# Optimization experiments

Measured on AMD Instinct MI355X. Metric: run time of the kernel, lower is better.

Reference implementation:

```python
import jax, jax.numpy as jnp
import numpy as np
from jax import lax

LENGTH = 9
PAD = LENGTH // 2          # 4
WIN_SIZE = LENGTH * LENGTH # 81
EPS = 1e-09
ALPHA = 0.01
PENALTY = 'l2'


def setup_inputs() -> dict:
    key = jax.random.key(0)
    k1, k2, k3 = jax.random.split(key, 3)
    B, C, H, W = 8, 1, 1024, 1024
    I = jax.random.normal(k1, (B, C, H, W), dtype=jnp.float32)
    J = jax.random.normal(k2, (B, C, H, W), dtype=jnp.float32)
    s = jax.random.normal(k3, (B, 2, H, W), dtype=jnp.float32)
    # buffer: all-ones box filter, shape [out=1, in=C, k, k]
    sum_filt = jnp.ones((1, C, LENGTH, LENGTH), dtype=jnp.float32)
    return {"I": I, "J": J, "s": s, "sum_filt": sum_filt}


def _box_conv(x, filt):
    # NCHW conv with 'same' padding (odd kernel), stride 1 -> [B,1,H,W]
    return lax.conv_general_dilated(
        x, filt, window_strides=(1, 1),
        padding=[(PAD, PAD), (PAD, PAD)],
        dimension_numbers=('NCHW', 'OIHW', 'NCHW'))


def _compute_local_sums(I, J, filt):
    I2, J2, IJ = I * I, J * J, I * J
    I_sum = _box_conv(I, filt)
    J_sum = _box_conv(J, filt)
    I2_sum = _box_conv(I2, filt)
    J2_sum = _box_conv(J2, filt)
    IJ_sum = _box_conv(IJ, filt)
    u_I = I_sum / WIN_SIZE
    u_J = J_sum / WIN_SIZE
    cross = IJ_sum - u_J * I_sum - u_I * J_sum + u_I * u_J * WIN_SIZE
    I_var = I2_sum - 2 * u_I * I_sum + u_I * u_I * WIN_SIZE
    J_var = J2_sum - 2 * u_J * J_sum + u_J * u_J * WIN_SIZE
    return I_var, J_var, cross


def _gradient_loss(s):
    dy = jnp.abs(s[:, :, 1:, :] - s[:, :, :-1, :])
    dx = jnp.abs(s[:, :, :, 1:] - s[:, :, :, :-1])
    if PENALTY == 'l2':
        dy = dy * dy
        dx = dx * dx
    return (jnp.mean(dx) + jnp.mean(dy)) / 2.0


def reference(I, J, s, sum_filt):
    I_var, J_var, cross = _compute_local_sums(I, J, sum_filt)
    cc = cross * cross / (I_var * J_var + EPS)
    ncc_loss = -jnp.mean(cc)
    smoothness_loss = _gradient_loss(s) * ALPHA
    total_loss = ncc_loss + smoothness_loss
    return (total_loss, ncc_loss, smoothness_loss)
```

## Files before the change

### kernel.cpp

```cpp
#include <hip/hip_runtime.h>

#define HH 1024
#define WW 1024
#define NB 8
#define TY 4
#define NCC_WAVES (NB * (HH / TY))
#define NCC_BLOCKS (NCC_WAVES / 4)
#define SM_BLOCKS 256
#define GRID (NCC_BLOCKS + SM_BLOCKS)
#define RW (1.0f / 81.0f)

template <int SGN>
__device__ __forceinline__ void vrow16(const float* __restrict__ Ib, const float* __restrict__ Jb,
                                       int y, int lane,
                                       float vI[16], float vJ[16],
                                       float vI2[16], float vJ2[16], float vIJ[16]) {
    if (y < 0 || y >= HH) return;
    const float4* Ir = (const float4*)(Ib + (size_t)y * WW) + 4 * lane;
    const float4* Jr = (const float4*)(Jb + (size_t)y * WW) + 4 * lane;
    float4 i4[4], j4[4];
#pragma unroll
    for (int k = 0; k < 4; ++k) i4[k] = Ir[k];
#pragma unroll
    for (int k = 0; k < 4; ++k) j4[k] = Jr[k];
#pragma unroll
    for (int k = 0; k < 4; ++k) {
        const float fi[4] = {i4[k].x, i4[k].y, i4[k].z, i4[k].w};
        const float fj[4] = {j4[k].x, j4[k].y, j4[k].z, j4[k].w};
#pragma unroll
        for (int e = 0; e < 4; ++e) {
            const int c = 4 * k + e;
            const float a = fi[e], b = fj[e];
            if (SGN > 0) {
                vI[c] += a; vJ[c] += b;
                vI2[c] = fmaf(a, a, vI2[c]);
                vJ2[c] = fmaf(b, b, vJ2[c]);
                vIJ[c] = fmaf(a, b, vIJ[c]);
            } else {
                vI[c] -= a; vJ[c] -= b;
                vI2[c] = fmaf(-a, a, vI2[c]);
                vJ2[c] = fmaf(-b, b, vJ2[c]);
                vIJ[c] = fmaf(-a, b, vIJ[c]);
            }
        }
    }
}

__global__ __launch_bounds__(256) void fused_kernel(const float* __restrict__ I,
                                                    const float* __restrict__ J,
                                                    const float* __restrict__ S,
                                                    float* __restrict__ ws) {
    __shared__ float red[8];
    const int bid = blockIdx.x;
    const int t = threadIdx.x;
    const int lane = t & 63;
    const int wid = t >> 6;

    if ((bid % 3) < 2) {
        const int nblk = (bid / 3) * 2 + (bid % 3);
        const int ss = nblk * 4 + wid;
        const int b = ss >> 8;
        const int y0 = (ss & 255) * TY;
        const float* Ib = I + (size_t)b * HH * WW;
        const float* Jb = J + (size_t)b * HH * WW;

        float vI[16], vJ[16], vI2[16], vJ2[16], vIJ[16];
#pragma unroll
        for (int c = 0; c < 16; ++c) { vI[c] = 0; vJ[c] = 0; vI2[c] = 0; vJ2[c] = 0; vIJ[c] = 0; }
        float ccacc = 0.f;

#pragma unroll
        for (int k = 0; k < 8; ++k)
            vrow16<1>(Ib, Jb, y0 - 4 + k, lane, vI, vJ, vI2, vJ2, vIJ);

#pragma unroll
        for (int k = 0; k < TY; ++k) {
            const int y = y0 + k;
            vrow16<1>(Ib, Jb, y + 4, lane, vI, vJ, vI2, vJ2, vIJ);

            float lI[4], lJ[4], lI2[4], lJ2[4], lIJ[4];
            float rI[4], rJ[4], rI2[4], rJ2[4], rIJ[4];
#pragma unroll
            for (int j = 0; j < 4; ++j) {
                lI[j] = __shfl_up(vI[12 + j], 1);
                lJ[j] = __shfl_up(vJ[12 + j], 1);
                lI2[j] = __shfl_up(vI2[12 + j], 1);
                lJ2[j] = __shfl_up(vJ2[12 + j], 1);
                lIJ[j] = __shfl_up(vIJ[12 + j], 1);
                rI[j] = __shfl_down(vI[j], 1);
                rJ[j] = __shfl_down(vJ[j], 1);
                rI2[j] = __shfl_down(vI2[j], 1);
                rJ2[j] = __shfl_down(vJ2[j], 1);
                rIJ[j] = __shfl_down(vIJ[j], 1);
            }
            if (lane == 0) {
#pragma unroll
                for (int j = 0; j < 4; ++j) { lI[j] = 0; lJ[j] = 0; lI2[j] = 0; lJ2[j] = 0; lIJ[j] = 0; }
            }
            if (lane == 63) {
#pragma unroll
                for (int j = 0; j < 4; ++j) { rI[j] = 0; rJ[j] = 0; rI2[j] = 0; rJ2[j] = 0; rIJ[j] = 0; }
            }

            float wI = lI[0] + lI[1] + lI[2] + lI[3] + vI[0] + vI[1] + vI[2] + vI[3] + vI[4];
            float wJ = lJ[0] + lJ[1] + lJ[2] + lJ[3] + vJ[0] + vJ[1] + vJ[2] + vJ[3] + vJ[4];
            float wI2 = lI2[0] + lI2[1] + lI2[2] + lI2[3] + vI2[0] + vI2[1] + vI2[2] + vI2[3] + vI2[4];
            float wJ2 = lJ2[0] + lJ2[1] + lJ2[2] + lJ2[3] + vJ2[0] + vJ2[1] + vJ2[2] + vJ2[3] + vJ2[4];
            float wIJ = lIJ[0] + lIJ[1] + lIJ[2] + lIJ[3] + vIJ[0] + vIJ[1] + vIJ[2] + vIJ[3] + vIJ[4];

#pragma unroll
            for (int c = 0; c < 16; ++c) {
                if (c > 0) {
                    const float aI = (c < 12) ? vI[c + 4] : rI[c - 12];
                    const float aJ = (c < 12) ? vJ[c + 4] : rJ[c - 12];
                    const float aI2 = (c < 12) ? vI2[c + 4] : rI2[c - 12];
                    const float aJ2 = (c < 12) ? vJ2[c + 4] : rJ2[c - 12];
                    const float aIJ = (c < 12) ? vIJ[c + 4] : rIJ[c - 12];
                    const float sI = (c >= 5) ? vI[c - 5] : lI[c - 1];
                    const float sJ = (c >= 5) ? vJ[c - 5] : lJ[c - 1];
                    const float sI2 = (c >= 5) ? vI2[c - 5] : lI2[c - 1];
                    const float sJ2 = (c >= 5) ? vJ2[c - 5] : lJ2[c - 1];
                    const float sIJ = (c >= 5) ? vIJ[c - 5] : lIJ[c - 1];
                    wI += aI - sI; wJ += aJ - sJ;
                    wI2 += aI2 - sI2; wJ2 += aJ2 - sJ2;
                    wIJ += aIJ - sIJ;
                }
                const float t1 = wI * wJ;
                const float cross = fmaf(-t1, RW, wIJ);
                const float t2 = wI * wI;
                const float Iv = fmaf(-t2, RW, wI2);
                const float t3 = wJ * wJ;
                const float Jv = fmaf(-t3, RW, wJ2);
                const float den = fmaf(Iv, Jv, 1e-9f);
                ccacc += cross * cross * __builtin_amdgcn_rcpf(den);
            }

            vrow16<-1>(Ib, Jb, y - 4, lane, vI, vJ, vI2, vJ2, vIJ);
        }

#pragma unroll
        for (int o = 32; o; o >>= 1) ccacc += __shfl_down(ccacc, o);
        if (lane == 0) red[wid] = ccacc;
        __syncthreads();
        if (t == 0) ws[nblk] = red[0] + red[1] + red[2] + red[3];
    } else {
        const int sb = bid / 3;
        const int r0 = sb * 64 + wid * 16;
        const float* base = S + (size_t)r0 * WW;
        float dxacc = 0.f, dyacc = 0.f;

        float4 v[4];
        {
            const float4* rp4 = (const float4*)base + 4 * lane;
#pragma unroll
            for (int k = 0; k < 4; ++k) v[k] = rp4[k];
        }
#pragma unroll 2
        for (int k = 0; k < 16; ++k) {
            const float f[16] = {v[0].x, v[0].y, v[0].z, v[0].w, v[1].x, v[1].y, v[1].z, v[1].w,
                                 v[2].x, v[2].y, v[2].z, v[2].w, v[3].x, v[3].y, v[3].z, v[3].w};
#pragma unroll
            for (int c = 0; c < 15; ++c) { const float d = f[c + 1] - f[c]; dxacc = fmaf(d, d, dxacc); }
            const float nb0 = __shfl_down(v[0].x, 1);
            if (lane < 63) { const float d = nb0 - f[15]; dxacc = fmaf(d, d, dxacc); }

            if (((r0 + k) & (HH - 1)) != HH - 1) {
                const float4* np4 = (const float4*)(base + (size_t)(k + 1) * WW) + 4 * lane;
                float4 nv[4];
#pragma unroll
                for (int q = 0; q < 4; ++q) nv[q] = np4[q];
#pragma unroll
                for (int q = 0; q < 4; ++q) {
                    const float e0 = nv[q].x - v[q].x, e1 = nv[q].y - v[q].y;
                    const float e2 = nv[q].z - v[q].z, e3 = nv[q].w - v[q].w;
                    dyacc = fmaf(e0, e0, dyacc); dyacc = fmaf(e1, e1, dyacc);
                    dyacc = fmaf(e2, e2, dyacc); dyacc = fmaf(e3, e3, dyacc);
                }
#pragma unroll
                for (int q = 0; q < 4; ++q) v[q] = nv[q];
            }
        }

#pragma unroll
        for (int o = 32; o; o >>= 1) {
            dxacc += __shfl_down(dxacc, o);
            dyacc += __shfl_down(dyacc, o);
        }
        if (lane == 0) { red[wid] = dxacc; red[4 + wid] = dyacc; }
        __syncthreads();
        if (t == 0) {
            ws[NCC_BLOCKS + sb] = red[0] + red[1] + red[2] + red[3];
            ws[NCC_BLOCKS + SM_BLOCKS + sb] = red[4] + red[5] + red[6] + red[7];
        }
    }
}

__global__ __launch_bounds__(256) void finalize_kernel(const float* __restrict__ ws,
                                                       float* __restrict__ out) {
    __shared__ double sd[256];
    __shared__ double res[3];
    const int t = threadIdx.x;
    double cc = 0.0, dx = 0.0, dy = 0.0;
    for (int i = t; i < NCC_BLOCKS; i += 256) cc += (double)ws[i];
    for (int i = t; i < SM_BLOCKS; i += 256) dx += (double)ws[NCC_BLOCKS + i];
    for (int i = t; i < SM_BLOCKS; i += 256) dy += (double)ws[NCC_BLOCKS + SM_BLOCKS + i];

    sd[t] = cc; __syncthreads();
    for (int s = 128; s; s >>= 1) { if (t < s) sd[t] += sd[t + s]; __syncthreads(); }
    if (t == 0) res[0] = sd[0];
    __syncthreads();
    sd[t] = dx; __syncthreads();
    for (int s = 128; s; s >>= 1) { if (t < s) sd[t] += sd[t + s]; __syncthreads(); }
    if (t == 0) res[1] = sd[0];
    __syncthreads();
    sd[t] = dy; __syncthreads();
    for (int s = 128; s; s >>= 1) { if (t < s) sd[t] += sd[t + s]; __syncthreads(); }
    if (t == 0) {
        res[2] = sd[0];
        const double ncc = -(res[0] / ((double)NB * 1.0 * HH * WW));
        const double mdx = res[1] / ((double)NB * 2.0 * HH * (WW - 1));
        const double mdy = res[2] / ((double)NB * 2.0 * (HH - 1) * WW);
        const double smooth = 0.01 * 0.5 * (mdx + mdy);
        out[0] = (float)(ncc + smooth);
        out[1] = (float)ncc;
        out[2] = (float)smooth;
    }
}

extern "C" void kernel_launch(void* const* d_in, const int* in_sizes, int n_in,
                              void* d_out, int out_size, void* d_ws, size_t ws_size,
                              hipStream_t stream) {
    const float* I = (const float*)d_in[0];
    const float* J = (const float*)d_in[1];
    const float* S = (const float*)d_in[2];
    float* ws = (float*)d_ws;
    float* out = (float*)d_out;

    fused_kernel<<<GRID, 256, 0, stream>>>(I, J, S, ws);
    finalize_kernel<<<1, 256, 0, stream>>>(ws, out);
}
```

Baseline: 175.8 us.

## Split NCC rows into column bands with halo lanes and taller row tiles

Result: slower. 230.0 us (+30.8%).

```diff
diff --git a/kernel.cpp b/kernel.cpp
--- a/kernel.cpp
+++ b/kernel.cpp
@@ -3,53 +3,55 @@
 #define HH 1024
 #define WW 1024
 #define NB 8
-#define TY 4
-#define NCC_WAVES (NB * (HH / TY))
+#define TY 16
+#define BANDS 4
+#define NCC_WAVES (NB * BANDS * (HH / TY))
 #define NCC_BLOCKS (NCC_WAVES / 4)
 #define SM_BLOCKS 256
 #define GRID (NCC_BLOCKS + SM_BLOCKS)
 #define RW (1.0f / 81.0f)
 
 template <int SGN>
-__device__ __forceinline__ void vrow16(const float* __restrict__ Ib, const float* __restrict__ Jb,
-                                       int y, int lane,
-                                       float vI[16], float vJ[16],
-                                       float vI2[16], float vJ2[16], float vIJ[16]) {
-    if (y < 0 || y >= HH) return;
-    const float4* Ir = (const float4*)(Ib + (size_t)y * WW) + 4 * lane;
-    const float4* Jr = (const float4*)(Jb + (size_t)y * WW) + 4 * lane;
-    float4 i4[4], j4[4];
-#pragma unroll
-    for (int k = 0; k < 4; ++k) i4[k] = Ir[k];
-#pragma unroll
-    for (int k = 0; k < 4; ++k) j4[k] = Jr[k];
-#pragma unroll
-    for (int k = 0; k < 4; ++k) {
-        const float fi[4] = {i4[k].x, i4[k].y, i4[k].z, i4[k].w};
-        const float fj[4] = {j4[k].x, j4[k].y, j4[k].z, j4[k].w};
-#pragma unroll
-        for (int e = 0; e < 4; ++e) {
-            const int c = 4 * k + e;
-            const float a = fi[e], b = fj[e];
-            if (SGN > 0) {
-                vI[c] += a; vJ[c] += b;
-                vI2[c] = fmaf(a, a, vI2[c]);
-                vJ2[c] = fmaf(b, b, vJ2[c]);
-                vIJ[c] = fmaf(a, b, vIJ[c]);
-            } else {
-                vI[c] -= a; vJ[c] -= b;
-                vI2[c] = fmaf(-a, a, vI2[c]);
-                vJ2[c] = fmaf(-b, b, vJ2[c]);
-                vIJ[c] = fmaf(-a, b, vIJ[c]);
-            }
+__device__ __forceinline__ void acc4(const float4 a, const float4 b,
+                                     float vI[4], float vJ[4],
+                                     float vI2[4], float vJ2[4], float vIJ[4]) {
+    const float fa[4] = {a.x, a.y, a.z, a.w};
+    const float fb[4] = {b.x, b.y, b.z, b.w};
+#pragma unroll
+    for (int c = 0; c < 4; ++c) {
+        const float x = fa[c], y = fb[c];
+        if (SGN > 0) {
+            vI[c] += x; vJ[c] += y;
+            vI2[c] = fmaf(x, x, vI2[c]);
+            vJ2[c] = fmaf(y, y, vJ2[c]);
+            vIJ[c] = fmaf(x, y, vIJ[c]);
+        } else {
+            vI[c] -= x; vJ[c] -= y;
+            vI2[c] = fmaf(-x, x, vI2[c]);
+            vJ2[c] = fmaf(-y, y, vJ2[c]);
+            vIJ[c] = fmaf(-x, y, vIJ[c]);
         }
     }
 }
 
-__global__ __launch_bounds__(256) void fused_kernel(const float* __restrict__ I,
-                                                    const float* __restrict__ J,
-                                                    const float* __restrict__ S,
-                                                    float* __restrict__ ws) {
+__device__ __forceinline__ void slide(int lane, const float v[4], const float h[4], float W[4]) {
+    float l0 = __shfl_up(v[0], 1), l1 = __shfl_up(v[1], 1);
+    float l2 = __shfl_up(v[2], 1), l3 = __shfl_up(v[3], 1);
+    float r0 = __shfl_down(v[0], 1), r1 = __shfl_down(v[1], 1);
+    float r2 = __shfl_down(v[2], 1), r3 = __shfl_down(v[3], 1);
+    if (lane == 0) { l0 = h[0]; l1 = h[1]; l2 = h[2]; l3 = h[3]; }
+    if (lane == 63) { r0 = h[0]; r1 = h[1]; r2 = h[2]; r3 = h[3]; }
+    float w = l0 + l1 + l2 + l3 + v[0] + v[1] + v[2] + v[3] + r0;
+    W[0] = w;
+    w += r1 - l0; W[1] = w;
+    w += r2 - l1; W[2] = w;
+    w += r3 - l2; W[3] = w;
+}
+
+__global__ __launch_bounds__(256, 4) void fused_kernel(const float* __restrict__ I,
+                                                       const float* __restrict__ J,
+                                                       const float* __restrict__ S,
+                                                       float* __restrict__ ws) {
     __shared__ float red[8];
     const int bid = blockIdx.x;
     const int t = threadIdx.x;
@@ -60,82 +62,83 @@
         const int nblk = (bid / 3) * 2 + (bid % 3);
         const int ss = nblk * 4 + wid;
         const int b = ss >> 8;
-        const int y0 = (ss & 255) * TY;
+        const int rem = ss & 255;
+        const int band = rem & 3;
+        const int y0 = (rem >> 2) * TY;
+        const int x0 = band * 256 + lane * 4;
         const float* Ib = I + (size_t)b * HH * WW;
         const float* Jb = J + (size_t)b * HH * WW;
 
-        float vI[16], vJ[16], vI2[16], vJ2[16], vIJ[16];
-#pragma unroll
-        for (int c = 0; c < 16; ++c) { vI[c] = 0; vJ[c] = 0; vI2[c] = 0; vJ2[c] = 0; vIJ[c] = 0; }
+        const bool haloL = (lane == 0) && (band > 0);
+        const bool haloR = (lane == 63) && (band < BANDS - 1);
+        const bool halo = haloL || haloR;
+        const int hx = x0 + (haloL ? -4 : 4);
+
+        float vI[4] = {0, 0, 0, 0}, vJ[4] = {0, 0, 0, 0};
+        float vI2[4] = {0, 0, 0, 0}, vJ2[4] = {0, 0, 0, 0}, vIJ[4] = {0, 0, 0, 0};
+        float hI[4] = {0, 0, 0, 0}, hJ[4] = {0, 0, 0, 0};
+        float hI2[4] = {0, 0, 0, 0}, hJ2[4] = {0, 0, 0, 0}, hIJ[4] = {0, 0, 0, 0};
         float ccacc = 0.f;
 
-#pragma unroll
-        for (int k = 0; k < 8; ++k)
-            vrow16<1>(Ib, Jb, y0 - 4 + k, lane, vI, vJ, vI2, vJ2, vIJ);
-
-#pragma unroll
+#pragma unroll 2
+        for (int k = 0; k < 8; ++k) {
+            const int y = y0 - 4 + k;
+            if (y < 0) continue;
+            const float* rowI = Ib + (size_t)y * WW;
+            const float* rowJ = Jb + (size_t)y * WW;
+            const float4 a = *(const float4*)(rowI + x0);
+            const float4 bb = *(const float4*)(rowJ + x0);
+            float4 ha{0, 0, 0, 0}, hb{0, 0, 0, 0};
+            if (halo) { ha = *(const float4*)(rowI + hx); hb = *(const float4*)(rowJ + hx); }
+            acc4<1>(a, bb, vI, vJ, vI2, vJ2, vIJ);
+            acc4<1>(ha, hb, hI, hJ, hI2, hJ2, hIJ);
+        }
+
+#pragma unroll 2
         for (int k = 0; k < TY; ++k) {
             const int y = y0 + k;
-            vrow16<1>(Ib, Jb, y + 4, lane, vI, vJ, vI2, vJ2, vIJ);
-
-            float lI[4], lJ[4], lI2[4], lJ2[4], lIJ[4];
-            float rI[4], rJ[4], rI2[4], rJ2[4], rIJ[4];
-#pragma unroll
-            for (int j = 0; j < 4; ++j) {
-                lI[j] = __shfl_up(vI[12 + j], 1);
-                lJ[j] = __shfl_up(vJ[12 + j], 1);
-                lI2[j] = __shfl_up(vI2[12 + j], 1);
-                lJ2[j] = __shfl_up(vJ2[12 + j], 1);
-                lIJ[j] = __shfl_up(vIJ[12 + j], 1);
-                rI[j] = __shfl_down(vI[j], 1);
-                rJ[j] = __shfl_down(vJ[j], 1);
-                rI2[j] = __shfl_down(vI2[j], 1);
-                rJ2[j] = __shfl_down(vJ2[j], 1);
-                rIJ[j] = __shfl_down(vIJ[j], 1);
-            }
-            if (lane == 0) {
-#pragma unroll
-                for (int j = 0; j < 4; ++j) { lI[j] = 0; lJ[j] = 0; lI2[j] = 0; lJ2[j] = 0; lIJ[j] = 0; }
-            }
-            if (lane == 63) {
-#pragma unroll
-                for (int j = 0; j < 4; ++j) { rI[j] = 0; rJ[j] = 0; rI2[j] = 0; rJ2[j] = 0; rIJ[j] = 0; }
-            }
-
-            float wI = lI[0] + lI[1] + lI[2] + lI[3] + vI[0] + vI[1] + vI[2] + vI[3] + vI[4];
-            float wJ = lJ[0] + lJ[1] + lJ[2] + lJ[3] + vJ[0] + vJ[1] + vJ[2] + vJ[3] + vJ[4];
-            float wI2 = lI2[0] + lI2[1] + lI2[2] + lI2[3] + vI2[0] + vI2[1] + vI2[2] + vI2[3] + vI2[4];
-            float wJ2 = lJ2[0] + lJ2[1] + lJ2[2] + lJ2[3] + vJ2[0] + vJ2[1] + vJ2[2] + vJ2[3] + vJ2[4];
-            float wIJ = lIJ[0] + lIJ[1] + lIJ[2] + lIJ[3] + vIJ[0] + vIJ[1] + vIJ[2] + vIJ[3] + vIJ[4];
-
-#pragma unroll
-            for (int c = 0; c < 16; ++c) {
-                if (c > 0) {
-                    const float aI = (c < 12) ? vI[c + 4] : rI[c - 12];
-                    const float aJ = (c < 12) ? vJ[c + 4] : rJ[c - 12];
-                    const float aI2 = (c < 12) ? vI2[c + 4] : rI2[c - 12];
-                    const float aJ2 = (c < 12) ? vJ2[c + 4] : rJ2[c - 12];
-                    const float aIJ = (c < 12) ? vIJ[c + 4] : rIJ[c - 12];
-                    const float sI = (c >= 5) ? vI[c - 5] : lI[c - 1];
-                    const float sJ = (c >= 5) ? vJ[c - 5] : lJ[c - 1];
-                    const float sI2 = (c >= 5) ? vI2[c - 5] : lI2[c - 1];
-                    const float sJ2 = (c >= 5) ? vJ2[c - 5] : lJ2[c - 1];
-                    const float sIJ = (c >= 5) ? vIJ[c - 5] : lIJ[c - 1];
-                    wI += aI - sI; wJ += aJ - sJ;
-                    wI2 += aI2 - sI2; wJ2 += aJ2 - sJ2;
-                    wIJ += aIJ - sIJ;
-                }
-                const float t1 = wI * wJ;
-                const float cross = fmaf(-t1, RW, wIJ);
-                const float t2 = wI * wI;
-                const float Iv = fmaf(-t2, RW, wI2);
-                const float t3 = wJ * wJ;
-                const float Jv = fmaf(-t3, RW, wJ2);
+            const int ya = y + 4, ys = y - 4;
+            const bool la = (ya < HH), ls = (ys >= 0);
+
+            float4 aI{0, 0, 0, 0}, aJ{0, 0, 0, 0}, haI{0, 0, 0, 0}, haJ{0, 0, 0, 0};
+            float4 sI{0, 0, 0, 0}, sJ{0, 0, 0, 0}, hsI{0, 0, 0, 0}, hsJ{0, 0, 0, 0};
+            if (la) {
+                const float* rowI = Ib + (size_t)ya * WW;
+                const float* rowJ = Jb + (size_t)ya * WW;
+                aI = *(const float4*)(rowI + x0);
+                aJ = *(const float4*)(rowJ + x0);
+                if (halo) { haI = *(const float4*)(rowI + hx); haJ = *(const float4*)(rowJ + hx); }
+            }
+            if (ls) {
+                const float* rowI = Ib + (size_t)ys * WW;
+                const float* rowJ = Jb + (size_t)ys * WW;
+                sI = *(const float4*)(rowI + x0);
+                sJ = *(const float4*)(rowJ + x0);
+                if (halo) { hsI = *(const float4*)(rowI + hx); hsJ = *(const float4*)(rowJ + hx); }
+            }
+
+            acc4<1>(aI, aJ, vI, vJ, vI2, vJ2, vIJ);
+            acc4<1>(haI, haJ, hI, hJ, hI2, hJ2, hIJ);
+
+            float W0[4], W1[4], W2[4], W3[4], W4[4];
+            slide(lane, vI, hI, W0);
+            slide(lane, vJ, hJ, W1);
+            slide(lane, vI2, hI2, W2);
+            slide(lane, vJ2, hJ2, W3);
+            slide(lane, vIJ, hIJ, W4);
+
+#pragma unroll
+            for (int c = 0; c < 4; ++c) {
+                const float Is = W0[c], Js = W1[c];
+                const float cross = fmaf(-Is * Js, RW, W4[c]);
+                const float Iv = fmaf(-Is * Is, RW, W2[c]);
+                const float Jv = fmaf(-Js * Js, RW, W3[c]);
                 const float den = fmaf(Iv, Jv, 1e-9f);
                 ccacc += cross * cross * __builtin_amdgcn_rcpf(den);
             }
 
-            vrow16<-1>(Ib, Jb, y - 4, lane, vI, vJ, vI2, vJ2, vIJ);
+            acc4<-1>(sI, sJ, vI, vJ, vI2, vJ2, vIJ);
+            acc4<-1>(hsI, hsJ, hI, hJ, hI2, hJ2, hIJ);
         }
 
 #pragma unroll
```
